# Performance work log

Hardware: AMD Instinct MI355X
Metric: run time of the kernel (lower is better)

Reference implementation:

```python
import jax, jax.numpy as jnp
import numpy as np

N_ATOMS = 100000
N_EDGES = 6400000
CUTOFF = 12.0
CUTOFF_SR = 2.0
CUTOFF_SQ = CUTOFF * CUTOFF
KEHALF = 7.199822675975274  # ASE kehalf, unit factors = 1


def poly6_switch(d, cutoff):
    # Poly6 smooth switch-off: 1 at d=0, 0 at d>=cutoff
    x = d / cutoff
    sw = 1.0 - 10.0 * x**3 + 15.0 * x**4 - 6.0 * x**5
    return jnp.where(d < cutoff, sw, jnp.zeros_like(sw))


def setup_inputs() -> dict:
    key = jax.random.key(0)
    k1, k2, k3, k4, k5 = jax.random.split(key, 5)
    atomic_charges = jax.random.normal(k1, (N_ATOMS,), dtype=jnp.float32) * 0.3
    atomic_dipoles = jax.random.normal(k2, (N_ATOMS,), dtype=jnp.float32) * 0.1
    # distances in (0.5, 13.5): some pairs inside short-range, some beyond cutoff
    distances = jax.random.uniform(k3, (N_EDGES,), dtype=jnp.float32) * 13.0 + 0.5
    idx_i = jax.random.randint(k4, (N_EDGES,), 0, N_ATOMS, dtype=jnp.int32)
    idx_j = jax.random.randint(k5, (N_EDGES,), 0, N_ATOMS, dtype=jnp.int32)
    return {
        "atomic_charges": atomic_charges,
        "atomic_dipoles": atomic_dipoles,
        "distances": distances,
        "idx_i": idx_i,
        "idx_j": idx_j,
    }


def reference(atomic_charges, atomic_dipoles, distances, idx_i, idx_j):
    # gather per-edge charges / dipoles
    qi = atomic_charges[idx_i]
    qj = atomic_charges[idx_j]
    di = atomic_dipoles[idx_i]
    dj = atomic_dipoles[idx_j]

    d = distances
    d_sh = jnp.sqrt(d * d + 1.0)  # shielded distance

    sw_off = poly6_switch(d, CUTOFF_SR)
    sw_on = 1.0 - sw_off

    # split_distance=True branch (cutoff != cutoff_short_range):
    # shifted-force Coulomb (charge-charge, ~1/d)
    E_ord_q = 1.0 / d + d / CUTOFF_SQ - 2.0 / CUTOFF
    E_sh_q = 1.0 / d_sh + d_sh / CUTOFF_SQ - 2.0 / CUTOFF
    E_q = KEHALF * qi * qj * (sw_off * E_sh_q + sw_on * E_ord_q)

    # dipole-dipole term (~1/d^3), same shielded/ordinary blending
    E_ord_d = 1.0 / d**3
    E_sh_d = 1.0 / d_sh**3
    E_d = KEHALF * di * dj * (sw_off * E_sh_d + sw_on * E_ord_d)

    E = E_q + E_d
    E = jnp.where(d <= CUTOFF, E, jnp.zeros_like(E))

    # scatter-sum per-edge energies to atoms
    return jax.ops.segment_sum(E, idx_i, num_segments=N_ATOMS)
```

## Files before the change

kernel.cpp:

```cpp
#include <hip/hip_runtime.h>
#include <hip/hip_bf16.h>
#include <hip/hip_fp16.h>

#define CUTOFF_C    12.0f
#define CUTOFF_SR_C 2.0f
#define CUTOFF_SQ_C 144.0f
#define KEHALF_C    7.199822675975274f

#define BLK1   1024

#define CH_SOLO 40000
#define CH_DUO  20000

__device__ __forceinline__ float edge_energy(float d, float qi, float qj,
                                             float di, float dj) {
    float inv_d   = __frcp_rn(d);
    float dsh     = __fsqrt_rn(fmaf(d, d, 1.0f));
    float inv_dsh = __frcp_rn(dsh);
    float x  = d * (1.0f / CUTOFF_SR_C);
    float x3 = x * x * x;
    float sw = fmaf(x3, fmaf(x, fmaf(x, -6.0f, 15.0f), -10.0f), 1.0f);
    float sw_off = (d < CUTOFF_SR_C) ? sw : 0.0f;
    float Eoq = inv_d   + fmaf(d,   (1.0f / CUTOFF_SQ_C), -(2.0f / CUTOFF_C));
    float Esq = inv_dsh + fmaf(dsh, (1.0f / CUTOFF_SQ_C), -(2.0f / CUTOFF_C));
    float Eq  = (KEHALF_C * qi * qj) * fmaf(sw_off, Esq - Eoq, Eoq);
    float Eod = inv_d * inv_d * inv_d;
    float Esd = inv_dsh * inv_dsh * inv_dsh;
    float Ed  = (KEHALF_C * di * dj) * fmaf(sw_off, Esd - Eod, Eod);
    return Eq + Ed;
}

__device__ __forceinline__ unsigned h2bits(__half2 h) {
    union { __half2 h; unsigned u; } c; c.h = h; return c.u;
}
__device__ __forceinline__ __half2 bits2h(unsigned u) {
    union { unsigned u; __half2 h; } c; c.u = u; return c.h;
}
template <typename T>
__device__ __forceinline__ auto atom_add_h2(T* p, T v, int)
    -> decltype(atomicAdd(p, v), void()) {
    atomicAdd(p, v);
}
template <typename T>
__device__ __forceinline__ void atom_add_h2(T* p, T v, long) {
    unsigned* u = (unsigned*)p;
    unsigned old = *u, assumed;
    do {
        assumed = old;
        __half2 sum = __hadd2(bits2h(assumed), v);
        old = atomicCAS(u, assumed, h2bits(sum));
    } while (old != assumed);
}

__device__ __forceinline__ unsigned vw_bits(float d, unsigned hqbits) {
    float inv_d   = __builtin_amdgcn_rcpf(d);
    float dsh2    = fmaf(d, d, 1.0f);
    float inv_dsh = __builtin_amdgcn_rsqf(dsh2);
    float dsh     = dsh2 * inv_dsh;
    float x  = d * (1.0f / CUTOFF_SR_C);
    float x3 = x * x * x;
    float sw = fmaf(x3, fmaf(x, fmaf(x, -6.0f, 15.0f), -10.0f), 1.0f);
    float sw_off = (d < CUTOFF_SR_C) ? sw : 0.0f;
    float Foq = inv_d   + fmaf(d,   (1.0f / CUTOFF_SQ_C), -(2.0f / CUTOFF_C));
    float Fsq = inv_dsh + fmaf(dsh, (1.0f / CUTOFF_SQ_C), -(2.0f / CUTOFF_C));
    float F   = fmaf(sw_off, Fsq - Foq, Foq);
    float God = inv_d * inv_d * inv_d;
    float Gsd = inv_dsh * inv_dsh * inv_dsh;
    float G   = fmaf(sw_off, Gsd - God, God);
    float2 q2 = __half22float2(bits2h(hqbits));
    __half2 vw = __floats2half2_rn((KEHALF_C * q2.x) * F, (KEHALF_C * q2.y) * G);
    return h2bits(vw);
}

__global__ __launch_bounds__(256) void pc_pack_qd_h(
    const float* __restrict__ q,
    const float* __restrict__ dip,
    __half2*     __restrict__ qd,
    int n_atoms)
{
    int a = blockIdx.x * 256 + threadIdx.x;
    if (a < n_atoms) qd[a] = __floats2half2_rn(q[a], dip[a]);
}

__global__ __launch_bounds__(256) void pc_edge_vw(
    const float*   __restrict__ dist,
    const int*     __restrict__ idx_j,
    const __half2* __restrict__ qd,
    uint4*         __restrict__ vwo,
    unsigned*      __restrict__ vws,
    int n_edges, int n4, int half)
{
    const int t = blockIdx.x * 256 + (int)threadIdx.x;
    const int4*   j4p = (const int4*)idx_j;
    const float4* d4p = (const float4*)dist;
    const __half2 hzero = __floats2half2_rn(0.0f, 0.0f);

    if (t < half) {
        const int  ga = t;
        const int  gb = t + half;
        const bool vb = gb < n4;
        const int  gbs = vb ? gb : ga;

        int4   ja = j4p[ga];
        int4   jb = j4p[gbs];
        float4 da = d4p[ga];
        float4 db = d4p[gbs];

        bool va0 = da.x <= CUTOFF_C, va1 = da.y <= CUTOFF_C;
        bool va2 = da.z <= CUTOFF_C, va3 = da.w <= CUTOFF_C;
        bool vb0 = db.x <= CUTOFF_C, vb1 = db.y <= CUTOFF_C;
        bool vb2 = db.z <= CUTOFF_C, vb3 = db.w <= CUTOFF_C;

        __half2 q0 = va0 ? qd[ja.x] : hzero;
        __half2 q1 = va1 ? qd[ja.y] : hzero;
        __half2 q2 = va2 ? qd[ja.z] : hzero;
        __half2 q3 = va3 ? qd[ja.w] : hzero;
        __half2 q4 = vb0 ? qd[jb.x] : hzero;
        __half2 q5 = vb1 ? qd[jb.y] : hzero;
        __half2 q6 = vb2 ? qd[jb.z] : hzero;
        __half2 q7 = vb3 ? qd[jb.w] : hzero;

        unsigned w0 = vw_bits(da.x, h2bits(q0));
        unsigned w1 = vw_bits(da.y, h2bits(q1));
        unsigned w2 = vw_bits(da.z, h2bits(q2));
        unsigned w3 = vw_bits(da.w, h2bits(q3));
        unsigned w4 = vw_bits(db.x, h2bits(q4));
        unsigned w5 = vw_bits(db.y, h2bits(q5));
        unsigned w6 = vw_bits(db.z, h2bits(q6));
        unsigned w7 = vw_bits(db.w, h2bits(q7));

        w0 = va0 ? w0 : 0u;  w1 = va1 ? w1 : 0u;
        w2 = va2 ? w2 : 0u;  w3 = va3 ? w3 : 0u;
        w4 = vb0 ? w4 : 0u;  w5 = vb1 ? w5 : 0u;
        w6 = vb2 ? w6 : 0u;  w7 = vb3 ? w7 : 0u;

        vwo[ga] = make_uint4(w0, w1, w2, w3);
        if (vb) vwo[gb] = make_uint4(w4, w5, w6, w7);
    }

    const int tl = n_edges & 3;
    if (blockIdx.x == 0 && (int)threadIdx.x < tl) {
        int e = (n4 << 2) + (int)threadIdx.x;
        float d = dist[e];
        bool  v = d <= CUTOFF_C;
        __half2 hq = v ? qd[idx_j[e]] : hzero;
        unsigned w = vw_bits(d, h2bits(hq));
        vws[e] = v ? w : 0u;
    }
}

template <int CH, int BLK>
__global__ __launch_bounds__(BLK) void pc_scatter_vw(
    const int*      __restrict__ idx_i,
    const unsigned* __restrict__ vw,
    __half2*        __restrict__ partial,
    int n_edges, int n4, int S, int gps, int n_atoms)
{
    extern __shared__ char smem[];
    __half2* acc2 = (__half2*)smem;

    const int s = blockIdx.x % S;
    const int c = blockIdx.x / S;
    const unsigned base = (unsigned)(c * CH);
    const int lim = min(CH, n_atoms - (int)base);

    {
        uint4* z4 = (uint4*)acc2;
        const uint4 z = make_uint4(0u, 0u, 0u, 0u);
        for (int i = threadIdx.x; i < CH / 4; i += BLK) z4[i] = z;
    }
    __syncthreads();

    const int4*  i4p = (const int4*)idx_i;
    const uint4* v4p = (const uint4*)vw;
    const int g0 = s * gps;
    const int g1 = min(g0 + gps, n4);
    for (int g = g0 + (int)threadIdx.x; g < g1; g += 2 * BLK) {
        const int  gB   = g + BLK;
        const bool hasB = gB < g1;
        const int  gBs  = hasB ? gB : g;

        int4  iA = i4p[g];
        int4  iB = i4p[gBs];
        uint4 vA = v4p[g];
        uint4 vB = v4p[gBs];

        unsigned a0 = (unsigned)iA.x - base;
        unsigned a1 = (unsigned)iA.y - base;
        unsigned a2 = (unsigned)iA.z - base;
        unsigned a3 = (unsigned)iA.w - base;
        if (a0 < (unsigned)CH) atom_add_h2(&acc2[a0], bits2h(vA.x), 0);
        if (a1 < (unsigned)CH) atom_add_h2(&acc2[a1], bits2h(vA.y), 0);
        if (a2 < (unsigned)CH) atom_add_h2(&acc2[a2], bits2h(vA.z), 0);
        if (a3 < (unsigned)CH) atom_add_h2(&acc2[a3], bits2h(vA.w), 0);
        if (hasB) {
            unsigned b0 = (unsigned)iB.x - base;
            unsigned b1 = (unsigned)iB.y - base;
            unsigned b2 = (unsigned)iB.z - base;
            unsigned b3 = (unsigned)iB.w - base;
            if (b0 < (unsigned)CH) atom_add_h2(&acc2[b0], bits2h(vB.x), 0);
            if (b1 < (unsigned)CH) atom_add_h2(&acc2[b1], bits2h(vB.y), 0);
            if (b2 < (unsigned)CH) atom_add_h2(&acc2[b2], bits2h(vB.z), 0);
            if (b3 < (unsigned)CH) atom_add_h2(&acc2[b3], bits2h(vB.w), 0);
        }
    }

    if (s == S - 1) {
        for (int e = (n4 << 2) + (int)threadIdx.x; e < n_edges; e += BLK) {
            unsigned lc = (unsigned)idx_i[e] - base;
            if (lc < (unsigned)CH) atom_add_h2(&acc2[lc], bits2h(vw[e]), 0);
        }
    }

    __syncthreads();
    __half2* row = partial + (size_t)s * n_atoms + (int)base;
    if (((n_atoms & 3) == 0) && (lim & 3) == 0) {
        uint4* r4 = (uint4*)row;
        const uint4* a4 = (const uint4*)acc2;
        for (int i = threadIdx.x; i < lim / 4; i += BLK) r4[i] = a4[i];
    } else {
        for (int i = threadIdx.x; i < lim; i += BLK) row[i] = acc2[i];
    }
}

__global__ __launch_bounds__(256) void pc_reduce_vw(
    const __half2* __restrict__ partial,
    const float*   __restrict__ q,
    const float*   __restrict__ dip,
    float*         __restrict__ out,
    int n_atoms, int S)
{
    __shared__ float2 sh[256];
    int a0   = blockIdx.x * 64;
    int lane = threadIdx.x & 63;
    int w    = threadIdx.x >> 6;
    int a    = a0 + lane;

    float sv = 0.0f, sw = 0.0f;
    if (a < n_atoms) {
        int per = S >> 2;
        const __half2* p = partial + a;
        int s = w * per, send = s + per;
        for (; s < send; ++s) {
            float2 t = __half22float2(p[(size_t)s * n_atoms]);
            sv += t.x; sw += t.y;
        }
    }
    sh[threadIdx.x] = make_float2(sv, sw);
    __syncthreads();
    if (w == 0 && a < n_atoms) {
        float2 t0 = sh[lane],       t1 = sh[64 + lane];
        float2 t2 = sh[128 + lane], t3 = sh[192 + lane];
        float fv = (t0.x + t1.x) + (t2.x + t3.x);
        float fw = (t0.y + t1.y) + (t2.y + t3.y);
        out[a] = fmaf(q[a], fv, dip[a] * fw);
    }
}

__global__ __launch_bounds__(256) void pc_dipole_edges_atomic(
    const float* __restrict__ q,
    const float* __restrict__ dip,
    const float* __restrict__ dist,
    const int*   __restrict__ idx_i,
    const int*   __restrict__ idx_j,
    float*       __restrict__ out,
    int n_edges)
{
    int t = blockIdx.x * blockDim.x + threadIdx.x;
    const int stride = gridDim.x * blockDim.x;
    for (int e = t; e < n_edges; e += stride) {
        float d = dist[e];
        if (d > CUTOFF_C) continue;
        int i = idx_i[e], j = idx_j[e];
        atomicAdd(&out[i], edge_energy(d, q[i], q[j], dip[i], dip[j]));
    }
}

static int probe_blocks(const void* f, int blk, size_t lds) {
    hipError_t e1 = hipFuncSetAttribute(
        f, hipFuncAttributeMaxDynamicSharedMemorySize, (int)lds);
    int nb = 0;
    hipError_t e2 = hipOccupancyMaxActiveBlocksPerMultiprocessor(&nb, f, blk, lds);
    if (e1 != hipSuccess || e2 != hipSuccess) return 0;
    return nb;
}

extern "C" void kernel_launch(void* const* d_in, const int* in_sizes, int n_in,
                              void* d_out, int out_size, void* d_ws, size_t ws_size,
                              hipStream_t stream) {
    const float* q     = (const float*)d_in[0];
    const float* dip   = (const float*)d_in[1];
    const float* dist  = (const float*)d_in[2];
    const int*   idx_i = (const int*)d_in[3];
    const int*   idx_j = (const int*)d_in[4];
    float*       out   = (float*)d_out;

    int n_edges = in_sizes[2];
    int n_atoms = out_size;
    int n4      = n_edges >> 2;
    int half    = (n4 + 1) >> 1;

    size_t qd_b = ((size_t)n_atoms * sizeof(__half2) + 255) & ~(size_t)255;
    size_t vw_b = (((size_t)n_edges * 4) + 255) & ~(size_t)255;

    size_t lds_solo = (size_t)CH_SOLO * sizeof(__half2);
    size_t lds_duo  = (size_t)CH_DUO  * sizeof(__half2);
    int nb_solo = probe_blocks((const void*)&pc_scatter_vw<CH_SOLO, BLK1>,
                               BLK1, lds_solo);
    int nb_duo  = probe_blocks((const void*)&pc_scatter_vw<CH_DUO, BLK1>,
                               BLK1, lds_duo);

    bool   use_solo = (nb_solo >= 1);
    int    CH  = use_solo ? CH_SOLO : CH_DUO;
    size_t lds = use_solo ? lds_solo : lds_duo;
    int    cap = use_solo ? 256 : 512;

    int S_new = 0, nch = 0;
    bool scatter_ok = (use_solo || nb_duo >= 2);
    if (scatter_ok && n_atoms > 0 && n4 > 0 && ws_size > qd_b + vw_b) {
        nch = (n_atoms + CH - 1) / CH;
        S_new = (cap / nch) & ~7;
        size_t avail = ws_size - qd_b - vw_b;
        int S_fit = (int)(avail / ((size_t)n_atoms * sizeof(__half2))) & ~7;
        if (S_fit < S_new) S_new = S_fit;
    }

    if (S_new >= 8) {
        __half2*  qd      = (__half2*)d_ws;
        unsigned* vw      = (unsigned*)((char*)d_ws + qd_b);
        __half2*  partial = (__half2*)((char*)d_ws + qd_b + vw_b);
        int       gps     = (n4 + S_new - 1) / S_new;
        int       gridA   = (half + 255) / 256;
        if (gridA < 1) gridA = 1;

        pc_pack_qd_h<<<(n_atoms + 255) / 256, 256, 0, stream>>>(q, dip, qd,
                                                                n_atoms);
        pc_edge_vw<<<gridA, 256, 0, stream>>>(dist, idx_j, qd,
                                              (uint4*)vw, vw,
                                              n_edges, n4, half);
        if (use_solo)
            pc_scatter_vw<CH_SOLO, BLK1>
                <<<S_new * nch, BLK1, lds, stream>>>(
                    idx_i, vw, partial, n_edges, n4, S_new, gps, n_atoms);
        else
            pc_scatter_vw<CH_DUO, BLK1>
                <<<S_new * nch, BLK1, lds, stream>>>(
                    idx_i, vw, partial, n_edges, n4, S_new, gps, n_atoms);
        pc_reduce_vw<<<(n_atoms + 63) / 64, 256, 0, stream>>>(
            partial, q, dip, out, n_atoms, S_new);
        return;
    }

    hipMemsetAsync(out, 0, (size_t)n_atoms * sizeof(float), stream);
    int grid = (n_edges + 255) / 256;
    if (grid < 1) grid = 1;
    pc_dipole_edges_atomic<<<grid, 256, 0, stream>>>(
        q, dip, dist, idx_i, idx_j, out, n_edges);
}
```

Baseline: 168.1 us.

## Fuse per-edge energy computation into chunked LDS scatter kernel

Removes the separate edge kernel that wrote a per-edge packed half2 value array. Each scatter block now reads dist, idx_i and idx_j directly and computes the energy term only for edges that are within the cutoff and fall in its atom chunk. This drops the intermediate array write and read and one launch. The cost is that every atom-chunk pass rereads an extra input stream. It also switches the default to the smaller-chunk, two-blocks-per-CU configuration, which raises the number of chunk passes over the edge data.

Result: faster. 152.4 us, median of 2 (-9.3%).

```diff
diff --git a/kernel.cpp b/kernel.cpp
--- a/kernel.cpp
+++ b/kernel.cpp
@@ -9,8 +9,8 @@
 
 #define BLK1   1024
 
+#define CH_DUO  20000
 #define CH_SOLO 40000
-#define CH_DUO  20000
 
 __device__ __forceinline__ float edge_energy(float d, float qi, float qj,
                                              float di, float dj) {
@@ -82,78 +82,13 @@
     if (a < n_atoms) qd[a] = __floats2half2_rn(q[a], dip[a]);
 }
 
-__global__ __launch_bounds__(256) void pc_edge_vw(
+template <int CH, int BLK>
+__global__ __launch_bounds__(BLK) void pc_fused_sc(
     const float*   __restrict__ dist,
+    const int*     __restrict__ idx_i,
     const int*     __restrict__ idx_j,
     const __half2* __restrict__ qd,
-    uint4*         __restrict__ vwo,
-    unsigned*      __restrict__ vws,
-    int n_edges, int n4, int half)
-{
-    const int t = blockIdx.x * 256 + (int)threadIdx.x;
-    const int4*   j4p = (const int4*)idx_j;
-    const float4* d4p = (const float4*)dist;
-    const __half2 hzero = __floats2half2_rn(0.0f, 0.0f);
-
-    if (t < half) {
-        const int  ga = t;
-        const int  gb = t + half;
-        const bool vb = gb < n4;
-        const int  gbs = vb ? gb : ga;
-
-        int4   ja = j4p[ga];
-        int4   jb = j4p[gbs];
-        float4 da = d4p[ga];
-        float4 db = d4p[gbs];
-
-        bool va0 = da.x <= CUTOFF_C, va1 = da.y <= CUTOFF_C;
-        bool va2 = da.z <= CUTOFF_C, va3 = da.w <= CUTOFF_C;
-        bool vb0 = db.x <= CUTOFF_C, vb1 = db.y <= CUTOFF_C;
-        bool vb2 = db.z <= CUTOFF_C, vb3 = db.w <= CUTOFF_C;
-
-        __half2 q0 = va0 ? qd[ja.x] : hzero;
-        __half2 q1 = va1 ? qd[ja.y] : hzero;
-        __half2 q2 = va2 ? qd[ja.z] : hzero;
-        __half2 q3 = va3 ? qd[ja.w] : hzero;
-        __half2 q4 = vb0 ? qd[jb.x] : hzero;
-        __half2 q5 = vb1 ? qd[jb.y] : hzero;
-        __half2 q6 = vb2 ? qd[jb.z] : hzero;
-        __half2 q7 = vb3 ? qd[jb.w] : hzero;
-
-        unsigned w0 = vw_bits(da.x, h2bits(q0));
-        unsigned w1 = vw_bits(da.y, h2bits(q1));
-        unsigned w2 = vw_bits(da.z, h2bits(q2));
-        unsigned w3 = vw_bits(da.w, h2bits(q3));
-        unsigned w4 = vw_bits(db.x, h2bits(q4));
-        unsigned w5 = vw_bits(db.y, h2bits(q5));
-        unsigned w6 = vw_bits(db.z, h2bits(q6));
-        unsigned w7 = vw_bits(db.w, h2bits(q7));
-
-        w0 = va0 ? w0 : 0u;  w1 = va1 ? w1 : 0u;
-        w2 = va2 ? w2 : 0u;  w3 = va3 ? w3 : 0u;
-        w4 = vb0 ? w4 : 0u;  w5 = vb1 ? w5 : 0u;
-        w6 = vb2 ? w6 : 0u;  w7 = vb3 ? w7 : 0u;
-
-        vwo[ga] = make_uint4(w0, w1, w2, w3);
-        if (vb) vwo[gb] = make_uint4(w4, w5, w6, w7);
-    }
-
-    const int tl = n_edges & 3;
-    if (blockIdx.x == 0 && (int)threadIdx.x < tl) {
-        int e = (n4 << 2) + (int)threadIdx.x;
-        float d = dist[e];
-        bool  v = d <= CUTOFF_C;
-        __half2 hq = v ? qd[idx_j[e]] : hzero;
-        unsigned w = vw_bits(d, h2bits(hq));
-        vws[e] = v ? w : 0u;
-    }
-}
-
-template <int CH, int BLK>
-__global__ __launch_bounds__(BLK) void pc_scatter_vw(
-    const int*      __restrict__ idx_i,
-    const unsigned* __restrict__ vw,
-    __half2*        __restrict__ partial,
+    __half2*       __restrict__ partial,
     int n_edges, int n4, int S, int gps, int n_atoms)
 {
     extern __shared__ char smem[];
@@ -171,8 +106,11 @@
     }
     __syncthreads();
 
-    const int4*  i4p = (const int4*)idx_i;
-    const uint4* v4p = (const uint4*)vw;
+    const int4*   i4p = (const int4*)idx_i;
+    const int4*   j4p = (const int4*)idx_j;
+    const float4* d4p = (const float4*)dist;
+    const __half2 hzero = __floats2half2_rn(0.0f, 0.0f);
+
     const int g0 = s * gps;
     const int g1 = min(g0 + gps, n4);
     for (int g = g0 + (int)threadIdx.x; g < g1; g += 2 * BLK) {
@@ -180,35 +118,58 @@
         const bool hasB = gB < g1;
         const int  gBs  = hasB ? gB : g;
 
-        int4  iA = i4p[g];
-        int4  iB = i4p[gBs];
-        uint4 vA = v4p[g];
-        uint4 vB = v4p[gBs];
+        int4   iA = i4p[g];
+        int4   iB = i4p[gBs];
+        int4   jA = j4p[g];
+        int4   jB = j4p[gBs];
+        float4 dA = d4p[g];
+        float4 dB = d4p[gBs];
 
         unsigned a0 = (unsigned)iA.x - base;
         unsigned a1 = (unsigned)iA.y - base;
         unsigned a2 = (unsigned)iA.z - base;
         unsigned a3 = (unsigned)iA.w - base;
-        if (a0 < (unsigned)CH) atom_add_h2(&acc2[a0], bits2h(vA.x), 0);
-        if (a1 < (unsigned)CH) atom_add_h2(&acc2[a1], bits2h(vA.y), 0);
-        if (a2 < (unsigned)CH) atom_add_h2(&acc2[a2], bits2h(vA.z), 0);
-        if (a3 < (unsigned)CH) atom_add_h2(&acc2[a3], bits2h(vA.w), 0);
-        if (hasB) {
-            unsigned b0 = (unsigned)iB.x - base;
-            unsigned b1 = (unsigned)iB.y - base;
-            unsigned b2 = (unsigned)iB.z - base;
-            unsigned b3 = (unsigned)iB.w - base;
-            if (b0 < (unsigned)CH) atom_add_h2(&acc2[b0], bits2h(vB.x), 0);
-            if (b1 < (unsigned)CH) atom_add_h2(&acc2[b1], bits2h(vB.y), 0);
-            if (b2 < (unsigned)CH) atom_add_h2(&acc2[b2], bits2h(vB.z), 0);
-            if (b3 < (unsigned)CH) atom_add_h2(&acc2[b3], bits2h(vB.w), 0);
-        }
+        unsigned b0 = (unsigned)iB.x - base;
+        unsigned b1 = (unsigned)iB.y - base;
+        unsigned b2 = (unsigned)iB.z - base;
+        unsigned b3 = (unsigned)iB.w - base;
+
+        bool vA0 = (a0 < (unsigned)CH) && (dA.x <= CUTOFF_C);
+        bool vA1 = (a1 < (unsigned)CH) && (dA.y <= CUTOFF_C);
+        bool vA2 = (a2 < (unsigned)CH) && (dA.z <= CUTOFF_C);
+        bool vA3 = (a3 < (unsigned)CH) && (dA.w <= CUTOFF_C);
+        bool vB0 = hasB && (b0 < (unsigned)CH) && (dB.x <= CUTOFF_C);
+        bool vB1 = hasB && (b1 < (unsigned)CH) && (dB.y <= CUTOFF_C);
+        bool vB2 = hasB && (b2 < (unsigned)CH) && (dB.z <= CUTOFF_C);
+        bool vB3 = hasB && (b3 < (unsigned)CH) && (dB.w <= CUTOFF_C);
+
+        __half2 q0 = vA0 ? qd[jA.x] : hzero;
+        __half2 q1 = vA1 ? qd[jA.y] : hzero;
+        __half2 q2 = vA2 ? qd[jA.z] : hzero;
+        __half2 q3 = vA3 ? qd[jA.w] : hzero;
+        __half2 q4 = vB0 ? qd[jB.x] : hzero;
+        __half2 q5 = vB1 ? qd[jB.y] : hzero;
+        __half2 q6 = vB2 ? qd[jB.z] : hzero;
+        __half2 q7 = vB3 ? qd[jB.w] : hzero;
+
+        if (vA0) atom_add_h2(&acc2[a0], bits2h(vw_bits(dA.x, h2bits(q0))), 0);
+        if (vA1) atom_add_h2(&acc2[a1], bits2h(vw_bits(dA.y, h2bits(q1))), 0);
+        if (vA2) atom_add_h2(&acc2[a2], bits2h(vw_bits(dA.z, h2bits(q2))), 0);
+        if (vA3) atom_add_h2(&acc2[a3], bits2h(vw_bits(dA.w, h2bits(q3))), 0);
+        if (vB0) atom_add_h2(&acc2[b0], bits2h(vw_bits(dB.x, h2bits(q4))), 0);
+        if (vB1) atom_add_h2(&acc2[b1], bits2h(vw_bits(dB.y, h2bits(q5))), 0);
+        if (vB2) atom_add_h2(&acc2[b2], bits2h(vw_bits(dB.z, h2bits(q6))), 0);
+        if (vB3) atom_add_h2(&acc2[b3], bits2h(vw_bits(dB.w, h2bits(q7))), 0);
     }
 
     if (s == S - 1) {
         for (int e = (n4 << 2) + (int)threadIdx.x; e < n_edges; e += BLK) {
             unsigned lc = (unsigned)idx_i[e] - base;
-            if (lc < (unsigned)CH) atom_add_h2(&acc2[lc], bits2h(vw[e]), 0);
+            float d = dist[e];
+            if (lc < (unsigned)CH && d <= CUTOFF_C) {
+                unsigned w = vw_bits(d, h2bits(qd[idx_j[e]]));
+                atom_add_h2(&acc2[lc], bits2h(w), 0);
+            }
         }
     }
 
@@ -298,56 +259,50 @@
     int n_edges = in_sizes[2];
     int n_atoms = out_size;
     int n4      = n_edges >> 2;
-    int half    = (n4 + 1) >> 1;
 
     size_t qd_b = ((size_t)n_atoms * sizeof(__half2) + 255) & ~(size_t)255;
-    size_t vw_b = (((size_t)n_edges * 4) + 255) & ~(size_t)255;
-
+
+    size_t lds_duo  = (size_t)CH_DUO  * sizeof(__half2);
     size_t lds_solo = (size_t)CH_SOLO * sizeof(__half2);
-    size_t lds_duo  = (size_t)CH_DUO  * sizeof(__half2);
-    int nb_solo = probe_blocks((const void*)&pc_scatter_vw<CH_SOLO, BLK1>,
+    int nb_duo  = probe_blocks((const void*)&pc_fused_sc<CH_DUO, BLK1>,
+                               BLK1, lds_duo);
+    int nb_solo = probe_blocks((const void*)&pc_fused_sc<CH_SOLO, BLK1>,
                                BLK1, lds_solo);
-    int nb_duo  = probe_blocks((const void*)&pc_scatter_vw<CH_DUO, BLK1>,
-                               BLK1, lds_duo);
-
-    bool   use_solo = (nb_solo >= 1);
-    int    CH  = use_solo ? CH_SOLO : CH_DUO;
-    size_t lds = use_solo ? lds_solo : lds_duo;
-    int    cap = use_solo ? 256 : 512;
-
-    int S_new = 0, nch = 0;
-    bool scatter_ok = (use_solo || nb_duo >= 2);
-    if (scatter_ok && n_atoms > 0 && n4 > 0 && ws_size > qd_b + vw_b) {
+
+    bool   use_duo = (nb_duo >= 2);
+    int    CH  = use_duo ? CH_DUO : CH_SOLO;
+    size_t lds = use_duo ? lds_duo : lds_solo;
+    int    cap = use_duo ? 512 : 256;
+
+    int S = 0, nch = 0;
+    bool ok = (use_duo || nb_solo >= 1);
+    if (ok && n_atoms > 0 && n4 > 0 && ws_size > qd_b) {
         nch = (n_atoms + CH - 1) / CH;
-        S_new = (cap / nch) & ~7;
-        size_t avail = ws_size - qd_b - vw_b;
+        S = (cap / nch) & ~7;
+        size_t avail = ws_size - qd_b;
         int S_fit = (int)(avail / ((size_t)n_atoms * sizeof(__half2))) & ~7;
-        if (S_fit < S_new) S_new = S_fit;
-    }
-
-    if (S_new >= 8) {
-        __half2*  qd      = (__half2*)d_ws;
-        unsigned* vw      = (unsigned*)((char*)d_ws + qd_b);
-        __half2*  partial = (__half2*)((char*)d_ws + qd_b + vw_b);
-        int       gps     = (n4 + S_new - 1) / S_new;
-        int       gridA   = (half + 255) / 256;
-        if (gridA < 1) gridA = 1;
+        if (S_fit < S) S = S_fit;
+    }
+
+    if (S >= 8) {
+        __half2* qd      = (__half2*)d_ws;
+        __half2* partial = (__half2*)((char*)d_ws + qd_b);
+        int      gps     = (n4 + S - 1) / S;
 
         pc_pack_qd_h<<<(n_atoms + 255) / 256, 256, 0, stream>>>(q, dip, qd,
                                                                 n_atoms);
-        pc_edge_vw<<<gridA, 256, 0, stream>>>(dist, idx_j, qd,
-                                              (uint4*)vw, vw,
-                                              n_edges, n4, half);
-        if (use_solo)
-            pc_scatter_vw<CH_SOLO, BLK1>
-                <<<S_new * nch, BLK1, lds, stream>>>(
-                    idx_i, vw, partial, n_edges, n4, S_new, gps, n_atoms);
+        if (use_duo)
+            pc_fused_sc<CH_DUO, BLK1>
+                <<<S * nch, BLK1, lds, stream>>>(
+                    dist, idx_i, idx_j, qd, partial, n_edges, n4, S, gps,
+                    n_atoms);
         else
-            pc_scatter_vw<CH_DUO, BLK1>
-                <<<S_new * nch, BLK1, lds, stream>>>(
-                    idx_i, vw, partial, n_edges, n4, S_new, gps, n_atoms);
+            pc_fused_sc<CH_SOLO, BLK1>
+                <<<S * nch, BLK1, lds, stream>>>(
+                    dist, idx_i, idx_j, qd, partial, n_edges, n4, S, gps,
+                    n_atoms);
         pc_reduce_vw<<<(n_atoms + 63) / 64, 256, 0, stream>>>(
-            partial, q, dip, out, n_atoms, S_new);
+            partial, q, dip, out, n_atoms, S);
         return;
     }
 
```
